# Performance work log

Hardware: AMD Instinct MI355X
Metric: run time of the kernel (lower is better)

Reference implementation:

```python
import jax, jax.numpy as jnp
import numpy as np
from jax import lax

B, CIN, D = 1, 32, 80      # batch, input channels (diffusion volumes), cube side
CE, CH, COUT = 64, 256, 6  # encoding feats, hidden feats, output feats (DTI components)
N = 200000                 # number of masked voxels
K = 3                      # FOVin


def _conv3d(x, w, b):
    # x: [B,C,D,H,W], w: [O,I,3,3,3], zero padding 1 (matches Conv3d(k=3, pad=1))
    y = lax.conv_general_dilated(x, w, window_strides=(1, 1, 1),
                                 padding=[(K // 2, K // 2)] * 3,
                                 dimension_numbers=('NCDHW', 'OIDHW', 'NCDHW'))
    return y + b[None, :, None, None, None]


def _conv1x1(x, w, b):
    # pointwise Conv1d: x [B,C,N], w [O,C], b [O]
    return jnp.einsum('oc,bcn->bon', w, x) + b[None, :, None]


def setup_inputs() -> dict:
    key = jax.random.key(0)
    ks = jax.random.split(key, 16)
    s3 = 1.0 / np.sqrt(CIN * K ** 3)
    return {
        'img_block': jax.random.normal(ks[0], (B, CIN, D, D, D), jnp.float32),
        'coords0': jax.random.randint(ks[1], (1, N), 0, D, jnp.int32),
        'coords1': jax.random.randint(ks[2], (1, N), 0, D, jnp.int32),
        'coords2': jax.random.randint(ks[3], (1, N), 0, D, jnp.int32),
        # encoder Conv3d weights (kaiming-ish scale)
        'w_enc1': jax.random.normal(ks[4], (CE, CIN, K, K, K), jnp.float32) * s3,
        'b_enc1': jax.random.normal(ks[5], (CE,), jnp.float32) * 0.01,
        'w_enc2': jax.random.normal(ks[6], (CE, CE, K, K, K), jnp.float32) * (1.0 / np.sqrt(CE * K ** 3)),
        'b_enc2': jax.random.normal(ks[7], (CE,), jnp.float32) * 0.01,
        # process stack 1x1 Conv1d weights
        'w_p1': jax.random.normal(ks[8], (CH, CE), jnp.float32) * (1.0 / np.sqrt(CE)),
        'b_p1': jax.random.normal(ks[9], (CH,), jnp.float32) * 0.01,
        'w_p2': jax.random.normal(ks[10], (CH, CH), jnp.float32) * (1.0 / np.sqrt(CH)),
        'b_p2': jax.random.normal(ks[11], (CH,), jnp.float32) * 0.01,
        'w_p3': jax.random.normal(ks[12], (64, CH), jnp.float32) * (1.0 / np.sqrt(CH)),
        'b_p3': jax.random.normal(ks[13], (64,), jnp.float32) * 0.01,
        'w_p4': jax.random.normal(ks[14], (COUT, 64), jnp.float32) * (1.0 / np.sqrt(64)),
        'b_p4': jax.random.normal(ks[15], (COUT,), jnp.float32) * 0.01,
    }


def reference(img_block, coords0, coords1, coords2,
              w_enc1, b_enc1, w_enc2, b_enc2,
              w_p1, b_p1, w_p2, b_p2, w_p3, b_p3, w_p4, b_p4):
    relu = jax.nn.relu
    # net_extrafea: two Conv3d(k=3,pad=1)+ReLU
    f = relu(_conv3d(img_block, w_enc1, b_enc1))
    f = relu(_conv3d(f, w_enc2, b_enc2))          # [B, CE, D, D, D]
    # gather masked voxels -> [B, CE, N]
    g = f[:, :, coords0[0], coords1[0], coords2[0]]
    # net_process (Dropout = identity in eval mode):
    h = relu(_conv1x1(g, w_p1, b_p1))             # [B, CH, N]
    h = relu(_conv1x1(h, w_p2, b_p2))             # [B, CH, N]
    # outermost_linear head: Conv1d(CH->64) then Conv1d(64->COUT), no nonlinearity
    h = _conv1x1(h, w_p3, b_p3)                   # [B, 64, N]
    out = _conv1x1(h, w_p4, b_p4)                 # [B, COUT, N]
    return out
```

## Files before the change

kernel.cpp:

```cpp
#include <hip/hip_runtime.h>
#include <hip/hip_bf16.h>

#define DD 80
#define CIN 32
#define PLANE (DD*DD)
#define VOX (DD*DD*DD)
#define NPTS 200000

typedef __attribute__((ext_vector_type(8))) short bf16x8;
typedef __attribute__((ext_vector_type(4))) float floatx4;

static __device__ __forceinline__ short f2bf(float v) {
    __hip_bfloat16 b = __float2bfloat16(v);
    return *(short*)&b;
}

static __device__ __forceinline__ void async_copy16(void* lds, const void* g) {
    __builtin_amdgcn_global_load_lds(
        (const __attribute__((address_space(1))) unsigned int*)g,
        (__attribute__((address_space(3))) unsigned int*)lds, 16, 0, 0);
}

__global__ void convert_weights(const float* __restrict__ w2,
                                const float* __restrict__ w_p1,
                                const float* __restrict__ w_p2,
                                const float* __restrict__ w_p3,
                                const float* __restrict__ w_e1,
                                short* __restrict__ wpb, short* __restrict__ w1b,
                                short* __restrict__ w2b, short* __restrict__ w3b,
                                short* __restrict__ wc1) {
    int i = blockIdx.x * 256 + threadIdx.x;
    if (i < 110592) {
        int oc = i / 1728, j = i - oc * 1728;
        int off = j >> 6, ic = j & 63;
        wpb[i] = f2bf(w2[oc * 1728 + ic * 27 + off]);
    } else if (i < 110592 + 16384) {
        int j = i - 110592;
        w1b[j] = f2bf(w_p1[j]);
    } else if (i < 110592 + 16384 + 65536) {
        int j = i - 110592 - 16384;
        w2b[j] = f2bf(w_p2[j]);
    } else if (i < 110592 + 16384 + 65536 + 16384) {
        int j = i - 110592 - 16384 - 65536;
        w3b[j] = f2bf(w_p3[j]);
    } else if (i < 110592 + 16384 + 65536 + 16384 + 55296) {
        int j = i - (110592 + 16384 + 65536 + 16384);
        int off = j / 2048, r = j - off * 2048;
        int oc = r >> 5, ic = r & 31;
        wc1[j] = f2bf(w_e1[(oc * 32 + ic) * 27 + off]);
    }
}

__global__ __launch_bounds__(256) void transpose_img(
    const float* __restrict__ img, short* __restrict__ img_t)
{
    int v = blockIdx.x * 256 + threadIdx.x;
    if (v >= VOX) return;
    short row[32];
    #pragma unroll
    for (int ic = 0; ic < 32; ic++)
        row[ic] = f2bf(img[(size_t)ic * VOX + v]);
    int4* dst = (int4*)(img_t + (size_t)v * 32);
    #pragma unroll
    for (int c = 0; c < 4; c++) dst[c] = ((int4*)row)[c];
}

__global__ __launch_bounds__(256) void conv1_mfma(
    const short* __restrict__ img_t, const short* __restrict__ wc1,
    const float* __restrict__ b1, const short* __restrict__ zeros,
    short* __restrict__ f1)
{
    __shared__ short Alds[3072 * 16 / 2];

    const int bh = blockIdx.x;
    const int d = bh / DD, h = bh - d * DD;
    const int tid = threadIdx.x;
    const int w = tid >> 6, lane = tid & 63;
    const int q = lane >> 4, lc = lane & 15;

    for (int i = 0; i < 12; i++) {
        int s = (w * 12 + i) * 64 + lane;
        int row = s >> 2, c = s & 3;
        int cs = c ^ (row & 3);
        int rr = row / 82, v = row - rr * 82;
        int dz = rr / 3, dyy = rr - dz * 3;
        int zz = d + dz - 1, yy = h + dyy - 1, ww = v - 1;
        const short* src = zeros;
        if (row < 738 && (unsigned)zz < DD && (unsigned)yy < DD && (unsigned)ww < DD)
            src = img_t + ((size_t)(zz * PLANE + yy * DD + ww)) * 32 + cs * 8;
        async_copy16(&Alds[(w * 12 + i) * 512], src);
    }
    __syncthreads();

    floatx4 acc[5];
    #pragma unroll
    for (int mt = 0; mt < 5; mt++) acc[mt] = (floatx4){0.f, 0.f, 0.f, 0.f};

    #pragma unroll 3
    for (int off = 0; off < 27; ++off) {
        const int dz = off / 9, rem = off - dz * 9;
        const int dy = rem / 3, dx = rem - dy * 3;
        const int rr = dz * 3 + dy;
        bf16x8 bfr = *(const bf16x8*)(wc1 + ((off * 64 + w * 16 + lc) << 5) + q * 8);
        #pragma unroll
        for (int mt = 0; mt < 5; mt++) {
            const int vv = rr * 82 + mt * 16 + lc + dx;
            bf16x8 afr = *(const bf16x8*)(&Alds[vv * 32 + ((q ^ (vv & 3)) << 3)]);
            acc[mt] = __builtin_amdgcn_mfma_f32_16x16x32_bf16(afr, bfr, acc[mt], 0, 0, 0);
        }
    }

    const int oc = w * 16 + lc;
    const float bias = b1[oc];
    const size_t vbase = (size_t)(d * DD + h) * DD;
    #pragma unroll
    for (int mt = 0; mt < 5; mt++) {
        #pragma unroll
        for (int r = 0; r < 4; r++) {
            const int m = mt * 16 + q * 4 + r;
            float v = acc[mt][r] + bias;
            f1[(vbase + m) * 64 + oc] = f2bf(v > 0.f ? v : 0.f);
        }
    }
}

__global__ __launch_bounds__(256) void conv2_mfma(
    const short* __restrict__ f1s, const short* __restrict__ wpb,
    const float* __restrict__ b2,
    const int* __restrict__ c0, const int* __restrict__ c1, const int* __restrict__ c2,
    __hip_bfloat16* __restrict__ g)
{
    __shared__ short Blds[2][512 * 8];

    const int tid = threadIdx.x;
    const int w = tid >> 6, lane = tid & 63;
    const int q = lane >> 4, lc = lane & 15;
    const int pw = blockIdx.x * 256 + w * 64;

    int rowbase[4];
    int rowmask[4];
    #pragma unroll
    for (int mt = 0; mt < 4; mt++) {
        int p = pw + mt * 16 + lc;
        if (p > NPTS - 1) p = NPTS - 1;
        int z = c0[p], y = c1[p], x = c2[p];
        rowbase[mt] = (z * PLANE + y * DD + x) * 64;
        int m = 0;
        #pragma unroll
        for (int off = 0; off < 27; off++) {
            int dz = off / 9, dy = (off / 3) % 3, dx = off % 3;
            int ok = ((unsigned)(z + dz - 1) < DD) & ((unsigned)(y + dy - 1) < DD) &
                     ((unsigned)(x + dx - 1) < DD);
            m |= ok << off;
        }
        rowmask[mt] = m;
    }

    floatx4 acc[4][4];
    #pragma unroll
    for (int mt = 0; mt < 4; mt++)
        #pragma unroll
        for (int nt = 0; nt < 4; nt++)
            acc[mt][nt] = (floatx4){0.f, 0.f, 0.f, 0.f};

    #pragma unroll
    for (int it = 0; it < 2; it++) {
        int sb = it * 256 + w * 64;
        int s = sb + lane;
        int oc = s >> 3, cs = (s & 7) ^ (oc & 7);
        async_copy16(&Blds[0][sb * 8], wpb + oc * 1728 + 0 * 64 + cs * 8);
    }
    __syncthreads();

    for (int off = 0; off < 27; ++off) {
        if (off + 1 < 27) {
            #pragma unroll
            for (int it = 0; it < 2; it++) {
                int sb = it * 256 + w * 64;
                int s = sb + lane;
                int oc = s >> 3, cs = (s & 7) ^ (oc & 7);
                async_copy16(&Blds[(off + 1) & 1][sb * 8],
                             wpb + oc * 1728 + (off + 1) * 64 + cs * 8);
            }
        }

        const int dz = off / 9, rem = off - dz * 9;
        const int dy = rem / 3, dx = rem - dy * 3;
        const int delta = ((dz - 1) * PLANE + (dy - 1) * DD + (dx - 1)) * 64;

        bf16x8 afr[4][2];
        #pragma unroll
        for (int mt = 0; mt < 4; mt++) {
            const int valid = (rowmask[mt] >> off) & 1;
            #pragma unroll
            for (int ks = 0; ks < 2; ks++) {
                bf16x8 v = (bf16x8)(short)0;
                if (valid)
                    v = *(const bf16x8*)(f1s + rowbase[mt] + delta + ks * 32 + q * 8);
                afr[mt][ks] = v;
            }
        }
        bf16x8 bfr[4][2];
        #pragma unroll
        for (int nt = 0; nt < 4; nt++) {
            const int oc = nt * 16 + lc;
            #pragma unroll
            for (int ks = 0; ks < 2; ks++) {
                const int slot = oc * 8 + ((ks * 4 + q) ^ (oc & 7));
                bfr[nt][ks] = *(const bf16x8*)(&Blds[off & 1][slot * 8]);
            }
        }

        #pragma unroll
        for (int ks = 0; ks < 2; ks++)
            #pragma unroll
            for (int mt = 0; mt < 4; mt++)
                #pragma unroll
                for (int nt = 0; nt < 4; nt++)
                    acc[mt][nt] = __builtin_amdgcn_mfma_f32_16x16x32_bf16(
                        afr[mt][ks], bfr[nt][ks], acc[mt][nt], 0, 0, 0);

        __syncthreads();
    }

    #pragma unroll
    for (int nt = 0; nt < 4; nt++) {
        const int oc = nt * 16 + lc;
        const float bias = b2[oc];
        #pragma unroll
        for (int mt = 0; mt < 4; mt++) {
            const int pt = pw + mt * 16 + q * 4;
            #pragma unroll
            for (int r = 0; r < 4; r++) {
                if (pt + r < NPTS) {
                    float v = acc[mt][nt][r] + bias;
                    g[(size_t)(pt + r) * 64 + oc] = __float2bfloat16(v > 0.f ? v : 0.f);
                }
            }
        }
    }
}

__global__ __launch_bounds__(256) void mlp_mfma(
    const __hip_bfloat16* __restrict__ g,
    const short* __restrict__ w1b, const float* __restrict__ bp1,
    const short* __restrict__ w2b, const float* __restrict__ bp2,
    const short* __restrict__ w3b, const float* __restrict__ bp3,
    const float* __restrict__ wp4, const float* __restrict__ bp4,
    float* __restrict__ out)
{
    __shared__ short bufA[64 * 256];
    __shared__ short bufB[64 * 256];
    float* h3f = (float*)bufB;

    const int tid = threadIdx.x;
    const int pb = blockIdx.x * 64;
    const int w = tid >> 6, lane = tid & 63;
    const int q = lane >> 4, lc = lane & 15;

    const short* gs = (const short*)g;
    #pragma unroll
    for (int it = 0; it < 2; it++) {
        int idx = it * 256 + tid;
        int r = idx >> 3, c = idx & 7;
        int4 v = *(const int4*)(gs + (size_t)(pb + r) * 64 + c * 8);
        *(int4*)(&bufA[r * 256 + (c ^ (r & 7)) * 8]) = v;
    }
    __syncthreads();

    {
        floatx4 acc[4][4];
        #pragma unroll
        for (int mt = 0; mt < 4; mt++)
            #pragma unroll
            for (int nt = 0; nt < 4; nt++)
                acc[mt][nt] = (floatx4){0.f, 0.f, 0.f, 0.f};

        #pragma unroll
        for (int ks = 0; ks < 2; ks++) {
            bf16x8 bfr[4];
            #pragma unroll
            for (int nt = 0; nt < 4; nt++)
                bfr[nt] = *(const bf16x8*)(w1b + (w * 64 + nt * 16 + lc) * 64 + ks * 32 + q * 8);
            const int c = ks * 4 + q;
            #pragma unroll
            for (int mt = 0; mt < 4; mt++) {
                const int m = mt * 16 + lc;
                bf16x8 afr = *(const bf16x8*)(&bufA[m * 256 + (c ^ (m & 7)) * 8]);
                #pragma unroll
                for (int nt = 0; nt < 4; nt++)
                    acc[mt][nt] = __builtin_amdgcn_mfma_f32_16x16x32_bf16(afr, bfr[nt], acc[mt][nt], 0, 0, 0);
            }
        }
        float bias[4];
        #pragma unroll
        for (int nt = 0; nt < 4; nt++) bias[nt] = bp1[w * 64 + nt * 16 + lc];
        #pragma unroll
        for (int mt = 0; mt < 4; mt++)
            #pragma unroll
            for (int nt = 0; nt < 4; nt++) {
                const int col = w * 64 + nt * 16 + lc;
                #pragma unroll
                for (int r = 0; r < 4; r++) {
                    const int m = mt * 16 + q * 4 + r;
                    float v = acc[mt][nt][r] + bias[nt];
                    v = v > 0.f ? v : 0.f;
                    bufB[m * 256 + (((col >> 3) ^ (m & 7)) * 8 + (col & 7))] = f2bf(v);
                }
            }
    }
    __syncthreads();

    {
        floatx4 acc[4][4];
        #pragma unroll
        for (int mt = 0; mt < 4; mt++)
            #pragma unroll
            for (int nt = 0; nt < 4; nt++)
                acc[mt][nt] = (floatx4){0.f, 0.f, 0.f, 0.f};

        #pragma unroll
        for (int ks = 0; ks < 8; ks++) {
            bf16x8 bfr[4];
            #pragma unroll
            for (int nt = 0; nt < 4; nt++)
                bfr[nt] = *(const bf16x8*)(w2b + (w * 64 + nt * 16 + lc) * 256 + ks * 32 + q * 8);
            const int c = ks * 4 + q;
            #pragma unroll
            for (int mt = 0; mt < 4; mt++) {
                const int m = mt * 16 + lc;
                const int pc = (c & 24) | ((c & 7) ^ (m & 7));
                bf16x8 afr = *(const bf16x8*)(&bufB[m * 256 + pc * 8]);
                #pragma unroll
                for (int nt = 0; nt < 4; nt++)
                    acc[mt][nt] = __builtin_amdgcn_mfma_f32_16x16x32_bf16(afr, bfr[nt], acc[mt][nt], 0, 0, 0);
            }
        }
        float bias[4];
        #pragma unroll
        for (int nt = 0; nt < 4; nt++) bias[nt] = bp2[w * 64 + nt * 16 + lc];
        __syncthreads();
        #pragma unroll
        for (int mt = 0; mt < 4; mt++)
            #pragma unroll
            for (int nt = 0; nt < 4; nt++) {
                const int col = w * 64 + nt * 16 + lc;
                #pragma unroll
                for (int r = 0; r < 4; r++) {
                    const int m = mt * 16 + q * 4 + r;
                    float v = acc[mt][nt][r] + bias[nt];
                    v = v > 0.f ? v : 0.f;
                    bufA[m * 256 + (((col >> 3) ^ (m & 7)) * 8 + (col & 7))] = f2bf(v);
                }
            }
    }
    __syncthreads();

    {
        floatx4 acc[4];
        #pragma unroll
        for (int mt = 0; mt < 4; mt++) acc[mt] = (floatx4){0.f, 0.f, 0.f, 0.f};

        #pragma unroll
        for (int ks = 0; ks < 8; ks++) {
            bf16x8 bfr = *(const bf16x8*)(w3b + (w * 16 + lc) * 256 + ks * 32 + q * 8);
            const int c = ks * 4 + q;
            #pragma unroll
            for (int mt = 0; mt < 4; mt++) {
                const int m = mt * 16 + lc;
                const int pc = (c & 24) | ((c & 7) ^ (m & 7));
                bf16x8 afr = *(const bf16x8*)(&bufA[m * 256 + pc * 8]);
                acc[mt] = __builtin_amdgcn_mfma_f32_16x16x32_bf16(afr, bfr, acc[mt], 0, 0, 0);
            }
        }
        const float bias = bp3[w * 16 + lc];
        const int col = w * 16 + lc;
        __syncthreads();
        #pragma unroll
        for (int mt = 0; mt < 4; mt++)
            #pragma unroll
            for (int r = 0; r < 4; r++) {
                const int m = mt * 16 + q * 4 + r;
                h3f[m * 65 + col] = acc[mt][r] + bias;
            }
    }
    __syncthreads();

    for (int e = tid; e < 384; e += 256) {
        int c = e >> 6, p = e & 63;
        float a = bp4[c];
        const float* wr = wp4 + c * 64;
        const float* xr = h3f + p * 65;
        #pragma unroll 8
        for (int k = 0; k < 64; k++) a += wr[k] * xr[k];
        out[(size_t)c * NPTS + pb + p] = a;
    }
}

extern "C" void kernel_launch(void* const* d_in, const int* in_sizes, int n_in,
                              void* d_out, int out_size, void* d_ws, size_t ws_size,
                              hipStream_t stream) {
    const float* img = (const float*)d_in[0];
    const int* c0 = (const int*)d_in[1];
    const int* c1 = (const int*)d_in[2];
    const int* c2 = (const int*)d_in[3];
    const float* w_enc1 = (const float*)d_in[4];
    const float* b_enc1 = (const float*)d_in[5];
    const float* w_enc2 = (const float*)d_in[6];
    const float* b_enc2 = (const float*)d_in[7];
    const float* w_p1 = (const float*)d_in[8];
    const float* b_p1 = (const float*)d_in[9];
    const float* w_p2 = (const float*)d_in[10];
    const float* b_p2 = (const float*)d_in[11];
    const float* w_p3 = (const float*)d_in[12];
    const float* b_p3 = (const float*)d_in[13];
    const float* w_p4 = (const float*)d_in[14];
    const float* b_p4 = (const float*)d_in[15];
    float* out = (float*)d_out;

    short* f1b = (short*)d_ws;
    short* wpb = f1b + (size_t)VOX * 64;
    short* w1b = wpb + 110592;
    short* w2b = w1b + 16384;
    short* w3b = w2b + 65536;
    short* gb  = w3b + 16384;
    short* img_t = gb + (size_t)NPTS * 64;
    short* wc1 = img_t + (size_t)VOX * 32;
    short* zeros = wc1 + 55296;

    hipMemsetAsync(zeros, 0, 64, stream);
    convert_weights<<<(264192 + 255) / 256, 256, 0, stream>>>(
        w_enc2, w_p1, w_p2, w_p3, w_enc1, wpb, w1b, w2b, w3b, wc1);
    transpose_img<<<(VOX + 255) / 256, 256, 0, stream>>>(img, img_t);
    conv1_mfma<<<DD * DD, 256, 0, stream>>>(img_t, wc1, b_enc1, zeros, f1b);
    conv2_mfma<<<(NPTS + 255) / 256, 256, 0, stream>>>(
        f1b, wpb, b_enc2, c0, c1, c2, (__hip_bfloat16*)gb);
    mlp_mfma<<<NPTS / 64, 256, 0, stream>>>(
        (const __hip_bfloat16*)gb, w1b, b_p1, w2b, b_p2, w3b, b_p3, w_p4, b_p4, out);
}
```

Before: 440.8 us.

## Bucket-sort gathered points by spatial cell and remap blocks per XCD for locality

Adds a counting sort of the 200k gather points into 8^3-voxel cells (histogram, scan, scatter kernels), so conv2 processes spatially clustered points and their 27-neighbour f1 reads share cache lines. It also remaps block IDs so that contiguous chunks of points land on the same XCD and its L2. Outputs are written back to each point's original index through the permutation. This adds three small kernels, a memset and atomics, and turns the output stores into scattered writes.

```diff
diff --git a/kernel.cpp b/kernel.cpp
--- a/kernel.cpp
+++ b/kernel.cpp
@@ -124,18 +124,66 @@
     }
 }
 
+__global__ __launch_bounds__(256) void hist_cells(
+    const int* __restrict__ c0, const int* __restrict__ c1, const int* __restrict__ c2,
+    int* __restrict__ hist)
+{
+    int p = blockIdx.x * 256 + threadIdx.x;
+    if (p >= NPTS) return;
+    int cell = (c0[p] >> 3) * 100 + (c1[p] >> 3) * 10 + (c2[p] >> 3);
+    atomicAdd(&hist[cell], 1);
+}
+
+__global__ __launch_bounds__(1024) void scan_cells(int* __restrict__ hist) {
+    __shared__ int a[1024], b[1024];
+    const int t = threadIdx.x;
+    int self = (t < 1000) ? hist[t] : 0;
+    a[t] = self;
+    __syncthreads();
+    int* src = a; int* dst = b;
+    for (int d = 1; d < 1024; d <<= 1) {
+        int v = src[t];
+        if (t >= d) v += src[t - d];
+        dst[t] = v;
+        __syncthreads();
+        int* tmp = src; src = dst; dst = tmp;
+    }
+    if (t < 1000) hist[t] = src[t] - self;
+}
+
+__global__ __launch_bounds__(256) void scatter_points(
+    const int* __restrict__ c0, const int* __restrict__ c1, const int* __restrict__ c2,
+    int* __restrict__ cellofs, int* __restrict__ perm, int* __restrict__ pcoord)
+{
+    int p = blockIdx.x * 256 + threadIdx.x;
+    if (p >= NPTS) return;
+    int z = c0[p], y = c1[p], x = c2[p];
+    int cell = (z >> 3) * 100 + (y >> 3) * 10 + (x >> 3);
+    int pos = atomicAdd(&cellofs[cell], 1);
+    perm[pos] = p;
+    pcoord[pos] = z | (y << 8) | (x << 16);
+}
+
 __global__ __launch_bounds__(256) void conv2_mfma(
     const short* __restrict__ f1s, const short* __restrict__ wpb,
     const float* __restrict__ b2,
-    const int* __restrict__ c0, const int* __restrict__ c1, const int* __restrict__ c2,
+    const int* __restrict__ perm, const int* __restrict__ pcoord,
     __hip_bfloat16* __restrict__ g)
 {
     __shared__ short Blds[2][512 * 8];
 
+    int bid = blockIdx.x;
+    {
+        const int nwg = gridDim.x;
+        const int qq = nwg >> 3, rr = nwg & 7;
+        const int xcd = bid & 7, i = bid >> 3;
+        bid = (xcd < rr ? xcd * (qq + 1) : rr * (qq + 1) + (xcd - rr) * qq) + i;
+    }
+
     const int tid = threadIdx.x;
     const int w = tid >> 6, lane = tid & 63;
     const int q = lane >> 4, lc = lane & 15;
-    const int pw = blockIdx.x * 256 + w * 64;
+    const int pw = bid * 256 + w * 64;
 
     int rowbase[4];
     int rowmask[4];
@@ -143,7 +191,8 @@
     for (int mt = 0; mt < 4; mt++) {
         int p = pw + mt * 16 + lc;
         if (p > NPTS - 1) p = NPTS - 1;
-        int z = c0[p], y = c1[p], x = c2[p];
+        int pc = pcoord[p];
+        int z = pc & 0xff, y = (pc >> 8) & 0xff, x = (pc >> 16) & 0xff;
         rowbase[mt] = (z * PLANE + y * DD + x) * 64;
         int m = 0;
         #pragma unroll
@@ -224,17 +273,21 @@
     }
 
     #pragma unroll
-    for (int nt = 0; nt < 4; nt++) {
-        const int oc = nt * 16 + lc;
-        const float bias = b2[oc];
-        #pragma unroll
-        for (int mt = 0; mt < 4; mt++) {
-            const int pt = pw + mt * 16 + q * 4;
+    for (int mt = 0; mt < 4; mt++) {
+        const int pt = pw + mt * 16 + q * 4;
+        int orig[4];
+        #pragma unroll
+        for (int r = 0; r < 4; r++)
+            orig[r] = (pt + r < NPTS) ? perm[pt + r] : -1;
+        #pragma unroll
+        for (int nt = 0; nt < 4; nt++) {
+            const int oc = nt * 16 + lc;
+            const float bias = b2[oc];
             #pragma unroll
             for (int r = 0; r < 4; r++) {
-                if (pt + r < NPTS) {
+                if (orig[r] >= 0) {
                     float v = acc[mt][nt][r] + bias;
-                    g[(size_t)(pt + r) * 64 + oc] = __float2bfloat16(v > 0.f ? v : 0.f);
+                    g[(size_t)orig[r] * 64 + oc] = __float2bfloat16(v > 0.f ? v : 0.f);
                 }
             }
         }
@@ -428,13 +481,23 @@
     short* wc1 = img_t + (size_t)VOX * 32;
     short* zeros = wc1 + 55296;
 
+    int* perm   = (int*)img_t;
+    int* pcoord = perm + NPTS;
+    int* hist   = pcoord + NPTS;
+
     hipMemsetAsync(zeros, 0, 64, stream);
     convert_weights<<<(264192 + 255) / 256, 256, 0, stream>>>(
         w_enc2, w_p1, w_p2, w_p3, w_enc1, wpb, w1b, w2b, w3b, wc1);
     transpose_img<<<(VOX + 255) / 256, 256, 0, stream>>>(img, img_t);
     conv1_mfma<<<DD * DD, 256, 0, stream>>>(img_t, wc1, b_enc1, zeros, f1b);
+
+    hipMemsetAsync(hist, 0, 1000 * sizeof(int), stream);
+    hist_cells<<<(NPTS + 255) / 256, 256, 0, stream>>>(c0, c1, c2, hist);
+    scan_cells<<<1, 1024, 0, stream>>>(hist);
+    scatter_points<<<(NPTS + 255) / 256, 256, 0, stream>>>(c0, c1, c2, hist, perm, pcoord);
+
     conv2_mfma<<<(NPTS + 255) / 256, 256, 0, stream>>>(
-        f1b, wpb, b_enc2, c0, c1, c2, (__hip_bfloat16*)gb);
+        f1b, wpb, b_enc2, perm, pcoord, (__hip_bfloat16*)gb);
     mlp_mfma<<<NPTS / 64, 256, 0, stream>>>(
         (const __hip_bfloat16*)gb, w1b, b_p1, w2b, b_p2, w3b, b_p3, w_p4, b_p4, out);
 }
```

New measurement: 535.6 us. 1.22x slower.

## Drop LDS staging in conv2, read weights from global, double-buffer gathered rows

Applied to the files above, without the earlier changes.

Conv2 weights are now laid out offset-major, so each offset's 64x64 slice is contiguous. The kernel reads weight fragments straight from global/L2 instead of staging them through LDS with async copies and per-offset barriers. The 27-offset loop is fully unrolled with two register buffers, so the gathered activation rows for the next offset load while the current MFMAs run. Out-of-bounds neighbours read from a zero buffer instead of a branch. This removes 27 block-wide syncs but adds redundant global weight reads per wave and raises register pressure.

```diff
diff --git a/kernel.cpp b/kernel.cpp
--- a/kernel.cpp
+++ b/kernel.cpp
@@ -31,8 +31,8 @@
                                 short* __restrict__ wc1) {
     int i = blockIdx.x * 256 + threadIdx.x;
     if (i < 110592) {
-        int oc = i / 1728, j = i - oc * 1728;
-        int off = j >> 6, ic = j & 63;
+        int off = i >> 12, r = i & 4095;
+        int oc = r >> 6, ic = r & 63;
         wpb[i] = f2bf(w2[oc * 1728 + ic * 27 + off]);
     } else if (i < 110592 + 16384) {
         int j = i - 110592;
@@ -128,23 +128,22 @@
     const short* __restrict__ f1s, const short* __restrict__ wpb,
     const float* __restrict__ b2,
     const int* __restrict__ c0, const int* __restrict__ c1, const int* __restrict__ c2,
+    const short* __restrict__ zeros,
     __hip_bfloat16* __restrict__ g)
 {
-    __shared__ short Blds[2][512 * 8];
-
     const int tid = threadIdx.x;
     const int w = tid >> 6, lane = tid & 63;
     const int q = lane >> 4, lc = lane & 15;
     const int pw = blockIdx.x * 256 + w * 64;
 
-    int rowbase[4];
+    const short* arow[4];
     int rowmask[4];
     #pragma unroll
     for (int mt = 0; mt < 4; mt++) {
         int p = pw + mt * 16 + lc;
         if (p > NPTS - 1) p = NPTS - 1;
         int z = c0[p], y = c1[p], x = c2[p];
-        rowbase[mt] = (z * PLANE + y * DD + x) * 64;
+        arow[mt] = f1s + (size_t)(z * PLANE + y * DD + x) * 64;
         int m = 0;
         #pragma unroll
         for (int off = 0; off < 27; off++) {
@@ -163,65 +162,56 @@
         for (int nt = 0; nt < 4; nt++)
             acc[mt][nt] = (floatx4){0.f, 0.f, 0.f, 0.f};
 
-    #pragma unroll
-    for (int it = 0; it < 2; it++) {
-        int sb = it * 256 + w * 64;
-        int s = sb + lane;
-        int oc = s >> 3, cs = (s & 7) ^ (oc & 7);
-        async_copy16(&Blds[0][sb * 8], wpb + oc * 1728 + 0 * 64 + cs * 8);
-    }
-    __syncthreads();
-
-    for (int off = 0; off < 27; ++off) {
-        if (off + 1 < 27) {
-            #pragma unroll
-            for (int it = 0; it < 2; it++) {
-                int sb = it * 256 + w * 64;
-                int s = sb + lane;
-                int oc = s >> 3, cs = (s & 7) ^ (oc & 7);
-                async_copy16(&Blds[(off + 1) & 1][sb * 8],
-                             wpb + oc * 1728 + (off + 1) * 64 + cs * 8);
-            }
-        }
-
-        const int dz = off / 9, rem = off - dz * 9;
-        const int dy = rem / 3, dx = rem - dy * 3;
-        const int delta = ((dz - 1) * PLANE + (dy - 1) * DD + (dx - 1)) * 64;
-
-        bf16x8 afr[4][2];
-        #pragma unroll
-        for (int mt = 0; mt < 4; mt++) {
-            const int valid = (rowmask[mt] >> off) & 1;
-            #pragma unroll
-            for (int ks = 0; ks < 2; ks++) {
-                bf16x8 v = (bf16x8)(short)0;
-                if (valid)
-                    v = *(const bf16x8*)(f1s + rowbase[mt] + delta + ks * 32 + q * 8);
-                afr[mt][ks] = v;
-            }
-        }
-        bf16x8 bfr[4][2];
-        #pragma unroll
-        for (int nt = 0; nt < 4; nt++) {
-            const int oc = nt * 16 + lc;
-            #pragma unroll
-            for (int ks = 0; ks < 2; ks++) {
-                const int slot = oc * 8 + ((ks * 4 + q) ^ (oc & 7));
-                bfr[nt][ks] = *(const bf16x8*)(&Blds[off & 1][slot * 8]);
-            }
-        }
-
-        #pragma unroll
-        for (int ks = 0; ks < 2; ks++)
-            #pragma unroll
-            for (int mt = 0; mt < 4; mt++)
-                #pragma unroll
-                for (int nt = 0; nt < 4; nt++)
-                    acc[mt][nt] = __builtin_amdgcn_mfma_f32_16x16x32_bf16(
-                        afr[mt][ks], bfr[nt][ks], acc[mt][nt], 0, 0, 0);
-
-        __syncthreads();
-    }
+    const short* zrs = zeros;
+
+#define LOAD_A(off, dst)                                                      \
+    {                                                                         \
+        const int dz_ = (off) / 9, rem_ = (off) - dz_ * 9;                    \
+        const int dy_ = rem_ / 3, dx_ = rem_ - dy_ * 3;                       \
+        const int delta_ = ((dz_ - 1) * PLANE + (dy_ - 1) * DD + (dx_ - 1)) * 64; \
+        _Pragma("unroll")                                                     \
+        for (int mt = 0; mt < 4; mt++) {                                      \
+            const short* src_ = ((rowmask[mt] >> (off)) & 1)                  \
+                                    ? arow[mt] + delta_ : zrs;                \
+            dst[mt][0] = *(const bf16x8*)(src_ + q * 8);                      \
+            dst[mt][1] = *(const bf16x8*)(src_ + 32 + q * 8);                 \
+        }                                                                     \
+    }
+
+#define DO_OFF(off, abuf)                                                     \
+    {                                                                         \
+        bf16x8 bfr[4][2];                                                     \
+        _Pragma("unroll")                                                     \
+        for (int nt = 0; nt < 4; nt++) {                                      \
+            const int oc_ = nt * 16 + lc;                                     \
+            _Pragma("unroll")                                                 \
+            for (int ks = 0; ks < 2; ks++)                                    \
+                bfr[nt][ks] = *(const bf16x8*)(wpb + ((off) << 12) +          \
+                                               oc_ * 64 + (ks * 4 + q) * 8);  \
+        }                                                                     \
+        _Pragma("unroll")                                                     \
+        for (int ks = 0; ks < 2; ks++)                                        \
+            _Pragma("unroll")                                                 \
+            for (int mt = 0; mt < 4; mt++)                                    \
+                _Pragma("unroll")                                             \
+                for (int nt = 0; nt < 4; nt++)                                \
+                    acc[mt][nt] = __builtin_amdgcn_mfma_f32_16x16x32_bf16(    \
+                        abuf[mt][ks], bfr[nt][ks], acc[mt][nt], 0, 0, 0);     \
+    }
+
+    bf16x8 A0[4][2], A1[4][2];
+    LOAD_A(0, A0)
+    #pragma unroll
+    for (int base = 0; base < 26; base += 2) {
+        LOAD_A(base + 1, A1)
+        DO_OFF(base, A0)
+        LOAD_A(base + 2, A0)
+        DO_OFF(base + 1, A1)
+    }
+    DO_OFF(26, A0)
+
+#undef LOAD_A
+#undef DO_OFF
 
     #pragma unroll
     for (int nt = 0; nt < 4; nt++) {
@@ -428,13 +418,13 @@
     short* wc1 = img_t + (size_t)VOX * 32;
     short* zeros = wc1 + 55296;
 
-    hipMemsetAsync(zeros, 0, 64, stream);
+    hipMemsetAsync(zeros, 0, 128, stream);
     convert_weights<<<(264192 + 255) / 256, 256, 0, stream>>>(
         w_enc2, w_p1, w_p2, w_p3, w_enc1, wpb, w1b, w2b, w3b, wc1);
     transpose_img<<<(VOX + 255) / 256, 256, 0, stream>>>(img, img_t);
     conv1_mfma<<<DD * DD, 256, 0, stream>>>(img_t, wc1, b_enc1, zeros, f1b);
     conv2_mfma<<<(NPTS + 255) / 256, 256, 0, stream>>>(
-        f1b, wpb, b_enc2, c0, c1, c2, (__hip_bfloat16*)gb);
+        f1b, wpb, b_enc2, c0, c1, c2, zeros, (__hip_bfloat16*)gb);
     mlp_mfma<<<NPTS / 64, 256, 0, stream>>>(
         (const __hip_bfloat16*)gb, w1b, b_p1, w2b, b_p2, w3b, b_p3, w_p4, b_p4, out);
 }
```

Measured after the change: 535.5 us. 1.21x slower.
